# Kernel optimization log

Measured on AMD Instinct MI355X. Metric: run time of the kernel, lower is better.

The kernel has to match this reference:

```python
import jax, jax.numpy as jnp
import numpy as np

B, N, S, CIN, COUT, GDIM = 4, 128, 8, 8, 8, 7  # batch, points, coset samples, channels, g_embed+2*q_embed


def setup_inputs() -> dict:
    key = jax.random.key(0)
    ks = jax.random.split(key, 8)
    pairwise_g = jax.random.normal(ks[0], (B, N, N, S, S, GDIM), jnp.float32)
    coset_functions = jax.random.normal(ks[1], (B, N, S, CIN), jnp.float32)
    mask = jax.random.bernoulli(ks[2], 0.9, (B, N, S))  # bool key mask (B,N,S)
    # per-channel SumKernel params: k_y = Linear(2->1), k_g = Linear(GDIM->1), stacked over CIN channels
    w_y = jax.random.normal(ks[3], (CIN, 2), jnp.float32) * 0.1
    b_y = jax.random.normal(ks[4], (CIN,), jnp.float32) * 0.1
    w_g = jax.random.normal(ks[5], (CIN, GDIM), jnp.float32) * 0.1
    b_g = jax.random.normal(ks[6], (CIN,), jnp.float32) * 0.1
    w_lin = jax.random.normal(ks[7], (COUT, CIN), jnp.float32) * (1.0 / np.sqrt(CIN))
    return {"pairwise_g": pairwise_g, "coset_functions": coset_functions, "mask": mask,
            "w_y": w_y, "b_y": b_y, "w_g": w_g, "b_g": b_g, "w_lin": w_lin}


def reference(pairwise_g, coset_functions, mask, w_y, b_y, w_g, b_g, w_lin):
    # Vectorized over the original per-channel Python loop: channel axis c.
    y = coset_functions  # (B, N, S, C)
    # k_g(pairwise_g) per channel + both biases: (B,i,j,s1,s2,C)
    logits = jnp.einsum('bijstg,cg->bijstc', pairwise_g, w_g) + (b_g + b_y)
    # k_y([y_1, y_2]): y_1 indexed by key (j, s2) -> weight w_y[:,0]; y_2 by query (i, s1) -> w_y[:,1]
    key_term = y * w_y[:, 0]   # (B, N, S, C)
    qry_term = y * w_y[:, 1]   # (B, N, S, C)
    logits = logits + key_term[:, None, :, None, :, :] + qry_term[:, :, None, :, None, :]
    # plain exp (original does NOT subtract a max), zero out masked keys (j, s2)
    att = jnp.where(mask[:, None, :, None, :, None], jnp.exp(logits), 0.0)
    att = att / att.sum(axis=(2, 4), keepdims=True)  # normalize over key dims
    # weighted sum of key values over (j, s2), residual add
    out = y + jnp.einsum('bijstc,bjtc->bisc', att, y)
    out = out * mask[..., None].astype(out.dtype)
    # output linear c_in -> c_out, no bias (torch Linear: x @ W.T)
    return out @ w_lin.T
```

## Files before the change

### kernel.cpp

```cpp
#include <hip/hip_runtime.h>


namespace {

constexpr int kN = 128, kS = 8, kC = 8, kO = 8, kG = 7;
constexpr int kSplit = 4;
constexpr int kBI = 4 * kN;
constexpr int JSTRIDE = 68;

__global__ __launch_bounds__(256, 4)
void emha_partial(const float* __restrict__ pg,
                  const float* __restrict__ y,
                  const int*   __restrict__ mask,
                  const float* __restrict__ w_y,
                  const float* __restrict__ w_g,
                  float*       __restrict__ ws)
{
    __shared__ float lds_kw[32 * JSTRIDE];
    __shared__ float lds_kv[32 * JSTRIDE];
    __shared__ float red[4][8][16];

    const int t     = threadIdx.x;
    const int blk   = blockIdx.x;
    const int split = blk & 3;
    const int bi    = blk >> 2;
    const int b     = bi >> 7;

    const float4* src = reinterpret_cast<const float4*>(
        pg + ((size_t)bi * 1024 + 256 * split + t) * 56);
    float4 pv[14];
#pragma unroll
    for (int q = 0; q < 14; ++q) pv[q] = src[q];

    float wg[kC][kG];
#pragma unroll
    for (int c = 0; c < kC; ++c)
#pragma unroll
        for (int g = 0; g < kG; ++g)
            wg[c][g] = w_g[c * kG + g];

    const float* yb = y    + b * (kN * kS * kC) + split * 2048;
    const int*   mb = mask + b * (kN * kS)      + split * 256;
    const float  wy0 = w_y[2 * (t & 7)];
#pragma unroll
    for (int k = 0; k < 8; ++k) {
        const int idx = t + k * 256;
        const float yv = yb[idx];
        const int   m  = mb[idx >> 3];
        const float kw = m ? __expf(yv * wy0) : 0.0f;
        const int off = (idx >> 6) * JSTRIDE + (idx & 63);
        lds_kw[off] = kw;
        lds_kv[off] = kw * yv;
    }
    __syncthreads();

    const int jl = t >> 3;
    const float* p = reinterpret_cast<const float*>(pv);
    float num[kC], den[kC];
#pragma unroll
    for (int c = 0; c < kC; ++c) { num[c] = 0.0f; den[c] = 0.0f; }

#pragma unroll
    for (int s2 = 0; s2 < kS; ++s2) {
        const int lo = jl * JSTRIDE + s2 * 8;
        const float4 kva = *reinterpret_cast<const float4*>(&lds_kv[lo]);
        const float4 kvb = *reinterpret_cast<const float4*>(&lds_kv[lo + 4]);
        const float4 kwa = *reinterpret_cast<const float4*>(&lds_kw[lo]);
        const float4 kwb = *reinterpret_cast<const float4*>(&lds_kw[lo + 4]);
        const float kv[8] = {kva.x, kva.y, kva.z, kva.w, kvb.x, kvb.y, kvb.z, kvb.w};
        const float kw[8] = {kwa.x, kwa.y, kwa.z, kwa.w, kwb.x, kwb.y, kwb.z, kwb.w};
#pragma unroll
        for (int c = 0; c < kC; ++c) {
            float d =      p[s2 * kG + 0] * wg[c][0];
            d = fmaf(p[s2 * kG + 1], wg[c][1], d);
            d = fmaf(p[s2 * kG + 2], wg[c][2], d);
            d = fmaf(p[s2 * kG + 3], wg[c][3], d);
            d = fmaf(p[s2 * kG + 4], wg[c][4], d);
            d = fmaf(p[s2 * kG + 5], wg[c][5], d);
            d = fmaf(p[s2 * kG + 6], wg[c][6], d);
            const float e = __expf(d);
            num[c] = fmaf(e, kv[c], num[c]);
            den[c] = fmaf(e, kw[c], den[c]);
        }
    }

#pragma unroll
    for (int c = 0; c < kC; ++c) {
        num[c] += __shfl_xor(num[c], 8);
        num[c] += __shfl_xor(num[c], 16);
        num[c] += __shfl_xor(num[c], 32);
        den[c] += __shfl_xor(den[c], 8);
        den[c] += __shfl_xor(den[c], 16);
        den[c] += __shfl_xor(den[c], 32);
    }
    const int wave = t >> 6;
    const int lane = t & 63;
    if (lane < 8) {
#pragma unroll
        for (int c = 0; c < kC; ++c) {
            red[wave][lane][c]     = num[c];
            red[wave][lane][c + 8] = den[c];
        }
    }
    __syncthreads();

    if (t < 128) {
        float v = 0.0f;
#pragma unroll
        for (int w = 0; w < 4; ++w) v += red[w][t >> 4][t & 15];
        ws[(size_t)(split * kBI + bi) * 128 + t] = v;
    }
}

__global__ __launch_bounds__(256)
void emha_finalize(const float* __restrict__ ws,
                   const float* __restrict__ y,
                   const int*   __restrict__ mask,
                   const float* __restrict__ w_lin,
                   float*       __restrict__ out)
{
    const int tid = blockIdx.x * 256 + threadIdx.x;
    const int bi  = tid >> 3;
    const int s1  = tid & 7;

    float4 n0 = {0,0,0,0}, n1 = {0,0,0,0}, d0 = {0,0,0,0}, d1 = {0,0,0,0};
#pragma unroll
    for (int s = 0; s < kSplit; ++s) {
        const float4* pp = reinterpret_cast<const float4*>(
            ws + (size_t)(s * kBI + bi) * 128 + s1 * 16);
        const float4 a = pp[0], bq = pp[1], cq = pp[2], dq = pp[3];
        n0.x += a.x;  n0.y += a.y;  n0.z += a.z;  n0.w += a.w;
        n1.x += bq.x; n1.y += bq.y; n1.z += bq.z; n1.w += bq.w;
        d0.x += cq.x; d0.y += cq.y; d0.z += cq.z; d0.w += cq.w;
        d1.x += dq.x; d1.y += dq.y; d1.z += dq.z; d1.w += dq.w;
    }
    const float nn[8] = {n0.x, n0.y, n0.z, n0.w, n1.x, n1.y, n1.z, n1.w};
    const float dd[8] = {d0.x, d0.y, d0.z, d0.w, d1.x, d1.y, d1.z, d1.w};

    const float* yrow = y + (size_t)bi * 64 + s1 * 8;
    const int m = mask[bi * 8 + s1];
    float ob[8];
#pragma unroll
    for (int c = 0; c < kC; ++c)
        ob[c] = m ? (yrow[c] + nn[c] / dd[c]) : 0.0f;

    float o[8];
#pragma unroll
    for (int oo = 0; oo < kO; ++oo) {
        float acc = 0.0f;
#pragma unroll
        for (int c = 0; c < kC; ++c)
            acc = fmaf(ob[c], w_lin[oo * kC + c], acc);
        o[oo] = acc;
    }
    float4* op = reinterpret_cast<float4*>(out + (size_t)bi * 64 + s1 * 8);
    op[0] = make_float4(o[0], o[1], o[2], o[3]);
    op[1] = make_float4(o[4], o[5], o[6], o[7]);
}

}

extern "C" void kernel_launch(void* const* d_in, const int* in_sizes, int n_in,
                              void* d_out, int out_size, void* d_ws, size_t ws_size,
                              hipStream_t stream)
{
    const float* pg    = (const float*)d_in[0];
    const float* y     = (const float*)d_in[1];
    const int*   mask  = (const int*)  d_in[2];
    const float* w_y   = (const float*)d_in[3];
    const float* w_g   = (const float*)d_in[5];
    const float* w_lin = (const float*)d_in[7];
    float* out = (float*)d_out;
    float* wsf = (float*)d_ws;

    emha_partial<<<kBI * kSplit, 256, 0, stream>>>(pg, y, mask, w_y, w_g, wsf);
    emha_finalize<<<16, 256, 0, stream>>>(wsf, y, mask, w_lin, out);
}
```

Before: 33.27 us.

## Double key-split and assign half a coset row per thread

Splits the key dimension into 8 blocks instead of 4, doubling grid size. Each thread now loads half of one (j,s1) row of pairwise_g (7 float4) and covers 4 of the 8 s2 values, with an extra shuffle to combine the two halves. This halves per-thread register load and work, aiming for more parallelism and better latency hiding. In exchange it adds more partial-sum writes and more reads in the finalize kernel.

```diff
diff --git a/kernel.cpp b/kernel.cpp
--- a/kernel.cpp
+++ b/kernel.cpp
@@ -4,8 +4,9 @@
 namespace {
 
 constexpr int kN = 128, kS = 8, kC = 8, kO = 8, kG = 7;
-constexpr int kSplit = 4;
+constexpr int kSplit = 8;
 constexpr int kBI = 4 * kN;
+constexpr int kJB = kN / kSplit;
 constexpr int JSTRIDE = 68;
 
 __global__ __launch_bounds__(256, 4)
@@ -16,21 +17,24 @@
                   const float* __restrict__ w_g,
                   float*       __restrict__ ws)
 {
-    __shared__ float lds_kw[32 * JSTRIDE];
-    __shared__ float lds_kv[32 * JSTRIDE];
+    __shared__ float lds_kw[kJB * JSTRIDE];
+    __shared__ float lds_kv[kJB * JSTRIDE];
     __shared__ float red[4][8][16];
 
     const int t     = threadIdx.x;
     const int blk   = blockIdx.x;
-    const int split = blk & 3;
-    const int bi    = blk >> 2;
+    const int split = blk & 7;
+    const int bi    = blk >> 3;
     const int b     = bi >> 7;
 
+    const int m = t >> 1;
+    const int h = t & 1;
+
     const float4* src = reinterpret_cast<const float4*>(
-        pg + ((size_t)bi * 1024 + 256 * split + t) * 56);
-    float4 pv[14];
+        pg + (size_t)bi * 57344 + (size_t)(split * 128 + m) * 56 + h * 28);
+    float4 buf[7];
 #pragma unroll
-    for (int q = 0; q < 14; ++q) pv[q] = src[q];
+    for (int q = 0; q < 7; ++q) buf[q] = src[q];
 
     float wg[kC][kG];
 #pragma unroll
@@ -39,30 +43,31 @@
         for (int g = 0; g < kG; ++g)
             wg[c][g] = w_g[c * kG + g];
 
-    const float* yb = y    + b * (kN * kS * kC) + split * 2048;
-    const int*   mb = mask + b * (kN * kS)      + split * 256;
+    const float* yb = y    + b * (kN * kS * kC);
+    const int*   mb = mask + b * (kN * kS);
     const float  wy0 = w_y[2 * (t & 7)];
 #pragma unroll
-    for (int k = 0; k < 8; ++k) {
-        const int idx = t + k * 256;
-        const float yv = yb[idx];
-        const int   m  = mb[idx >> 3];
-        const float kw = m ? __expf(yv * wy0) : 0.0f;
+    for (int k = 0; k < 4; ++k) {
+        const int idx  = t + k * 256;
+        const int gidx = split * 1024 + idx;
+        const float yv = yb[gidx];
+        const int   mm = mb[gidx >> 3];
+        const float kwv = mm ? __expf(yv * wy0) : 0.0f;
         const int off = (idx >> 6) * JSTRIDE + (idx & 63);
-        lds_kw[off] = kw;
-        lds_kv[off] = kw * yv;
+        lds_kw[off] = kwv;
+        lds_kv[off] = kwv * yv;
     }
     __syncthreads();
 
-    const int jl = t >> 3;
-    const float* p = reinterpret_cast<const float*>(pv);
+    const int jl = m >> 3;
+    const float* pf = reinterpret_cast<const float*>(buf);
     float num[kC], den[kC];
 #pragma unroll
     for (int c = 0; c < kC; ++c) { num[c] = 0.0f; den[c] = 0.0f; }
 
 #pragma unroll
-    for (int s2 = 0; s2 < kS; ++s2) {
-        const int lo = jl * JSTRIDE + s2 * 8;
+    for (int s2i = 0; s2i < 4; ++s2i) {
+        const int lo = jl * JSTRIDE + (h * 4 + s2i) * 8;
         const float4 kva = *reinterpret_cast<const float4*>(&lds_kv[lo]);
         const float4 kvb = *reinterpret_cast<const float4*>(&lds_kv[lo + 4]);
         const float4 kwa = *reinterpret_cast<const float4*>(&lds_kw[lo]);
@@ -71,13 +76,13 @@
         const float kw[8] = {kwa.x, kwa.y, kwa.z, kwa.w, kwb.x, kwb.y, kwb.z, kwb.w};
 #pragma unroll
         for (int c = 0; c < kC; ++c) {
-            float d =      p[s2 * kG + 0] * wg[c][0];
-            d = fmaf(p[s2 * kG + 1], wg[c][1], d);
-            d = fmaf(p[s2 * kG + 2], wg[c][2], d);
-            d = fmaf(p[s2 * kG + 3], wg[c][3], d);
-            d = fmaf(p[s2 * kG + 4], wg[c][4], d);
-            d = fmaf(p[s2 * kG + 5], wg[c][5], d);
-            d = fmaf(p[s2 * kG + 6], wg[c][6], d);
+            float d =      pf[s2i * kG + 0] * wg[c][0];
+            d = fmaf(pf[s2i * kG + 1], wg[c][1], d);
+            d = fmaf(pf[s2i * kG + 2], wg[c][2], d);
+            d = fmaf(pf[s2i * kG + 3], wg[c][3], d);
+            d = fmaf(pf[s2i * kG + 4], wg[c][4], d);
+            d = fmaf(pf[s2i * kG + 5], wg[c][5], d);
+            d = fmaf(pf[s2i * kG + 6], wg[c][6], d);
             const float e = __expf(d);
             num[c] = fmaf(e, kv[c], num[c]);
             den[c] = fmaf(e, kw[c], den[c]);
@@ -86,20 +91,21 @@
 
 #pragma unroll
     for (int c = 0; c < kC; ++c) {
-        num[c] += __shfl_xor(num[c], 8);
+        num[c] += __shfl_xor(num[c], 1);
         num[c] += __shfl_xor(num[c], 16);
         num[c] += __shfl_xor(num[c], 32);
-        den[c] += __shfl_xor(den[c], 8);
+        den[c] += __shfl_xor(den[c], 1);
         den[c] += __shfl_xor(den[c], 16);
         den[c] += __shfl_xor(den[c], 32);
     }
-    const int wave = t >> 6;
+    const int w    = t >> 6;
     const int lane = t & 63;
-    if (lane < 8) {
+    if (lane < 16 && (lane & 1) == 0) {
+        const int s1 = lane >> 1;
 #pragma unroll
         for (int c = 0; c < kC; ++c) {
-            red[wave][lane][c]     = num[c];
-            red[wave][lane][c + 8] = den[c];
+            red[w][s1][c]     = num[c];
+            red[w][s1][c + 8] = den[c];
         }
     }
     __syncthreads();
@@ -107,7 +113,7 @@
     if (t < 128) {
         float v = 0.0f;
 #pragma unroll
-        for (int w = 0; w < 4; ++w) v += red[w][t >> 4][t & 15];
+        for (int ww = 0; ww < 4; ++ww) v += red[ww][t >> 4][t & 15];
         ws[(size_t)(split * kBI + bi) * 128 + t] = v;
     }
 }
@@ -138,11 +144,11 @@
     const float dd[8] = {d0.x, d0.y, d0.z, d0.w, d1.x, d1.y, d1.z, d1.w};
 
     const float* yrow = y + (size_t)bi * 64 + s1 * 8;
-    const int m = mask[bi * 8 + s1];
+    const int mq = mask[bi * 8 + s1];
     float ob[8];
 #pragma unroll
     for (int c = 0; c < kC; ++c)
-        ob[c] = m ? (yrow[c] + nn[c] / dd[c]) : 0.0f;
+        ob[c] = mq ? (yrow[c] + nn[c] / dd[c]) : 0.0f;
 
     float o[8];
 #pragma unroll
```

Measured after the change: 31.85 us. 1.04x faster.
